# Kernel tuning notes

Measured on AMD Instinct MI355X. Metric: run time of the kernel, lower is better.

Reference implementation:

```python
import jax, jax.numpy as jnp
import numpy as np

B, L1, L2 = 4, 1024, 512
D_PG, D_EX = 2304, 1024
H, HKV, DH = 8, 4, 256
SCALE = 256.0 ** -0.5


def _rope(x, cos, sin):
    # x: [B, L, h, DH]; cos/sin: [B, L, 1, DH//2]
    x = x.astype(jnp.float32)
    x1, x2 = jnp.split(x, 2, axis=-1)
    return jnp.concatenate([x1 * cos - x2 * sin, x2 * cos + x1 * sin], axis=-1)


def setup_inputs() -> dict:
    key = jax.random.key(0)
    ks = jax.random.split(key, 16)
    s = 0.02
    return {
        "pg_embeds": jax.random.normal(ks[0], (B, L1, D_PG), jnp.float32),
        "ex_embeds": jax.random.normal(ks[1], (B, L2, D_EX), jnp.float32),
        "cos": jax.random.normal(ks[2], (B, L1 + L2, 1, DH // 2), jnp.float32),
        "sin": jax.random.normal(ks[3], (B, L1 + L2, 1, DH // 2), jnp.float32),
        "attention_mask": jnp.zeros((B, L1 + L2, L1 + L2), jnp.float32),
        "Wq0": jax.random.normal(ks[4], (H * DH, D_PG), jnp.float32) * s,
        "Wk0": jax.random.normal(ks[5], (HKV * DH, D_PG), jnp.float32) * s,
        "Wv0": jax.random.normal(ks[6], (HKV * DH, D_PG), jnp.float32) * s,
        "Wo0": jax.random.normal(ks[7], (D_PG, H * DH), jnp.float32) * s,
        "Wq1": jax.random.normal(ks[8], (H * DH, D_EX), jnp.float32) * s,
        "Wk1": jax.random.normal(ks[9], (HKV * DH, D_EX), jnp.float32) * s,
        "Wv1": jax.random.normal(ks[10], (HKV * DH, D_EX), jnp.float32) * s,
        "Wo1": jax.random.normal(ks[11], (D_EX, H * DH), jnp.float32) * s,
    }


def reference(pg_embeds, ex_embeds, cos, sin, attention_mask,
              Wq0, Wk0, Wv0, Wo0, Wq1, Wk1, Wv1, Wo1):
    b, l1 = pg_embeds.shape[0], pg_embeds.shape[1]
    l2 = ex_embeds.shape[1]
    # per-stream QKV projections, then concat along sequence
    q = jnp.concatenate([
        (pg_embeds @ Wq0.T).reshape(b, l1, H, DH),
        (ex_embeds @ Wq1.T).reshape(b, l2, H, DH)], axis=1)
    k = jnp.concatenate([
        (pg_embeds @ Wk0.T).reshape(b, l1, HKV, DH),
        (ex_embeds @ Wk1.T).reshape(b, l2, HKV, DH)], axis=1)
    v = jnp.concatenate([
        (pg_embeds @ Wv0.T).reshape(b, l1, HKV, DH),
        (ex_embeds @ Wv1.T).reshape(b, l2, HKV, DH)], axis=1)
    q = _rope(q, cos, sin)  # fp32
    k = _rope(k, cos, sin)
    # GQA: repeat KV heads to match query heads
    rep = H // HKV
    k = jnp.repeat(k, rep, axis=2)
    v = jnp.repeat(jnp.repeat(v, rep, axis=2).astype(jnp.float32), 1, axis=0)
    # scores: [B, H, L, L]
    scores = jnp.einsum('bqhd,bkhd->bhqk', q, k) * SCALE
    scores = scores + attention_mask[:, None, :, :]
    p = jax.nn.softmax(scores, axis=-1)
    att = jnp.einsum('bhqk,bkhd->bqhd', p, v).reshape(b, l1 + l2, H * DH)
    out0 = att[:, :l1] @ Wo0.T
    out1 = att[:, l1:] @ Wo1.T
    return (out0, out1)
```

## Files before the change

kernel.cpp:

```cpp
#include <hip/hip_runtime.h>
#include <stdint.h>
#include <stddef.h>


typedef _Float16 f16;
typedef _Float16 f16x8 __attribute__((ext_vector_type(8)));
typedef _Float16 f16x4 __attribute__((ext_vector_type(4)));
typedef float    f32x4 __attribute__((ext_vector_type(4)));

__device__ __forceinline__ void async_ld16(const void* g, void* l) {
  __builtin_amdgcn_global_load_lds((const __attribute__((address_space(1))) void*)g,
                                   (__attribute__((address_space(3))) void*)l,
                                   16, 0, 0);
}

template <typename Epi>
__device__ __forceinline__ void gemm256(f16* lds,
    const f16* __restrict__ A, int lda,
    const f16* __restrict__ B, int ldb,
    int K, Epi&& epi)
{
  const int t    = threadIdx.x;
  const int w    = t >> 6;
  const int lane = t & 63;
  const int q4   = lane >> 4;
  const int l16  = lane & 15;
  const int wm   = w >> 2;
  const int wn   = w & 3;

  f16* ldsA = lds;
  f16* ldsB = lds + 32768;

  const int scx = ((lane & 3) ^ ((lane >> 3) & 3)) * 8;
  const f16* aP = A + (size_t)(lane >> 2) * lda + scx;
  const f16* bP = B + (size_t)(lane >> 2) * ldb + scx;
  const size_t aR0 = (size_t)(w * 32) * lda;
  const size_t aR1 = aR0 + (size_t)16 * lda;
  const size_t bR0 = (size_t)(w * 32) * ldb;
  const size_t bR1 = bR0 + (size_t)16 * ldb;
  const int wo = w * 1024;

  const int sx = (l16 >> 1) & 3;
  const int arow = (wm * 128 + l16) * 32 + ((q4 ^ sx) * 8);
  const int brow = (wn * 64 + l16) * 32 + ((q4 ^ sx) * 8);

  f32x4 acc[8][4];
  const f32x4 vz = {0.f, 0.f, 0.f, 0.f};
#pragma unroll
  for (int i = 0; i < 8; ++i)
#pragma unroll
    for (int j = 0; j < 4; ++j) acc[i][j] = vz;

#pragma unroll
  for (int s = 0; s < 2; ++s) {
    const int kk = s * 32;
    async_ld16(aP + aR0 + kk, ldsA + s * 8192 + wo);
    async_ld16(aP + aR1 + kk, ldsA + s * 8192 + wo + 512);
    async_ld16(bP + bR0 + kk, ldsB + s * 8192 + wo);
    async_ld16(bP + bR1 + kk, ldsB + s * 8192 + wo + 512);
  }

  const int NT = K >> 6;
  for (int tk = 0; tk < NT; ++tk) {
    const int d  = (tk & 1) ? 16384 : 0;
    const int dn = 16384 - d;
    const bool st = tk + 1 < NT;
    const int kn = (tk + 1) << 6;
#pragma unroll
    for (int s = 0; s < 2; ++s) {
      if (s == 0 || st) asm volatile("s_waitcnt vmcnt(4)" ::: "memory");
      else              asm volatile("s_waitcnt vmcnt(0)" ::: "memory");
      asm volatile("s_barrier" ::: "memory");
      const f16* aS = ldsA + d + s * 8192;
      const f16* bS = ldsB + d + s * 8192;
      f16x8 af[8], bf[4];
#pragma unroll
      for (int i = 0; i < 8; ++i) af[i] = *(const f16x8*)(aS + arow + i * 512);
#pragma unroll
      for (int i = 0; i < 4; ++i) bf[i] = *(const f16x8*)(bS + brow + i * 512);
      if (st) {
        const int kk = kn + s * 32;
        async_ld16(aP + aR0 + kk, ldsA + dn + s * 8192 + wo);
        async_ld16(aP + aR1 + kk, ldsA + dn + s * 8192 + wo + 512);
        async_ld16(bP + bR0 + kk, ldsB + dn + s * 8192 + wo);
        async_ld16(bP + bR1 + kk, ldsB + dn + s * 8192 + wo + 512);
      }
      __builtin_amdgcn_s_setprio(1);
#pragma unroll
      for (int mi = 0; mi < 8; ++mi)
#pragma unroll
        for (int ni = 0; ni < 4; ++ni)
          acc[mi][ni] = __builtin_amdgcn_mfma_f32_16x16x32_f16(af[mi], bf[ni], acc[mi][ni], 0, 0, 0);
      __builtin_amdgcn_s_setprio(0);
      asm volatile("s_barrier" ::: "memory");
    }
  }

#pragma unroll
  for (int mi = 0; mi < 8; ++mi)
#pragma unroll
    for (int ni = 0; ni < 4; ++ni)
#pragma unroll
      for (int r = 0; r < 4; ++r)
        epi(wm * 128 + mi * 16 + q4 * 4 + r, wn * 64 + ni * 16 + l16, acc[mi][ni][r]);
}

template <typename Epi>
__device__ __forceinline__ void gemm_pipe(f16* lds,
    const f16* __restrict__ A, int lda,
    const f16* __restrict__ B, int ldb,
    int K, Epi&& epi)
{
  const int t    = threadIdx.x;
  const int w    = t >> 6;
  const int lane = t & 63;
  const int q4   = lane >> 4;
  const int l16  = lane & 15;
  const int wm   = w >> 1;
  const int wn   = w & 1;

  const int srow = w * 16 + (lane >> 2);
  const int scol = ((lane & 3) ^ ((lane >> 3) & 3)) * 8;
  const f16* aP = A + (size_t)srow * lda + scol;
  const f16* bP = B + (size_t)srow * ldb + scol;
  const size_t a128 = (size_t)128 * lda;
  const int wl = w * 512;

  const int sx = (l16 >> 1) & 3;
  const int arow = (wm * 64 + l16) * 32 + ((q4 ^ sx) * 8);
  const int brow = (wn * 64 + l16) * 32 + ((q4 ^ sx) * 8);

  f32x4 acc[4][4];
  const f32x4 vz = {0.f, 0.f, 0.f, 0.f};
#pragma unroll
  for (int i = 0; i < 4; ++i)
#pragma unroll
    for (int j = 0; j < 4; ++j) acc[i][j] = vz;

  async_ld16(aP,             lds + wl);
  async_ld16(aP + a128,      lds + 4096 + wl);
  async_ld16(bP,             lds + 32768 + wl);
  asm volatile("" ::: "memory");
  async_ld16(aP + 32,        lds + 8192 + wl);
  async_ld16(aP + a128 + 32, lds + 8192 + 4096 + wl);
  async_ld16(bP + 32,        lds + 32768 + 4096 + wl);
  asm volatile("s_waitcnt vmcnt(3)" ::: "memory");
  asm volatile("s_barrier" ::: "memory");

  const int NT = K >> 6;
  int cb = 0;
  for (int tk = 0; tk < NT; ++tk) {
    f16* aT = lds + cb * 16384;
    f16* bT = lds + 32768 + cb * 8192;
    f16* aD = lds + (cb ^ 1) * 16384;
    f16* bD = lds + 32768 + (cb ^ 1) * 8192;
    const int kn = (tk + 1) << 6;
    const bool st = tk < NT - 1;
#pragma unroll
    for (int s = 0; s < 2; ++s) {
      const f16* aS = aT + s * 8192;
      const f16* bS = bT + s * 4096;
      f16x8 af[4], bf[4];
#pragma unroll
      for (int i = 0; i < 4; ++i) {
        af[i] = *(const f16x8*)(aS + arow + i * 512);
        bf[i] = *(const f16x8*)(bS + brow + i * 512);
      }
      if (st) {
        if (s == 0) {
          async_ld16(aP + kn,        aD + wl);
          async_ld16(aP + a128 + kn, aD + 4096 + wl);
          async_ld16(bP + kn,        bD + wl);
        } else {
          async_ld16(aP + kn + 32,        aD + 8192 + wl);
          async_ld16(aP + a128 + kn + 32, aD + 8192 + 4096 + wl);
          async_ld16(bP + kn + 32,        bD + 4096 + wl);
        }
        asm volatile("s_waitcnt vmcnt(3)" ::: "memory");
      } else if (s == 0) {
        asm volatile("s_waitcnt vmcnt(0)" ::: "memory");
      }
      asm volatile("s_barrier" ::: "memory");
      __builtin_amdgcn_s_setprio(1);
#pragma unroll
      for (int mi = 0; mi < 4; ++mi)
#pragma unroll
        for (int ni = 0; ni < 4; ++ni)
          acc[mi][ni] = __builtin_amdgcn_mfma_f32_16x16x32_f16(af[mi], bf[ni], acc[mi][ni], 0, 0, 0);
      __builtin_amdgcn_s_setprio(0);
      asm volatile("s_barrier" ::: "memory");
    }
    cb ^= 1;
  }

#pragma unroll
  for (int mi = 0; mi < 4; ++mi)
#pragma unroll
    for (int ni = 0; ni < 4; ++ni)
#pragma unroll
      for (int r = 0; r < 4; ++r)
        epi(wm * 64 + mi * 16 + q4 * 4 + r, wn * 64 + ni * 16 + l16, acc[mi][ni][r]);
}

__global__ __launch_bounds__(512, 2) void k_qkv5(
    const f16* __restrict__ xpg, const f16* __restrict__ xex,
    const f16* __restrict__ W0,  const f16* __restrict__ W1,
    f16* __restrict__ q, f16* __restrict__ k, f16* __restrict__ v)
{
  __shared__ alignas(16) f16 lds[65536];
  const int idx = blockIdx.x;
  int by, bx, K; const f16 *A, *B;
  const bool s0 = idx < 256;
  if (s0) { by = idx >> 4; bx = idx & 15; K = 2304;
            A = xpg + (size_t)by * 256 * 2304; B = W0 + (size_t)bx * 256 * 2304; }
  else    { int j = idx - 256; by = j >> 4; bx = j & 15; K = 1024;
            A = xex + (size_t)by * 256 * 1024; B = W1 + (size_t)bx * 256 * 1024; }

  f16* D; int ldd, coff;
  if (bx < 8)       { D = q; ldd = 2048; coff = 0; }
  else if (bx < 12) { D = k; ldd = 1024; coff = 2048; }
  else              { D = v; ldd = 1024; coff = 3072; }
  const int colb = bx * 256 - coff;
  const int rowb = s0 ? ((by >> 2) * 1536 + (by & 3) * 256)
                      : ((by >> 1) * 1536 + 1024 + (by & 1) * 256);

  gemm256(lds, A, K, B, K, K, [&](int r, int c, float fv) {
    D[(size_t)(rowb + r) * ldd + colb + c] = (f16)fv;
  });
}

__global__ __launch_bounds__(256) void k_post(
    f16* __restrict__ q, f16* __restrict__ k,
    const float* __restrict__ cs, const float* __restrict__ sn,
    const float* __restrict__ msk, f16* __restrict__ mkh,
    const f16* __restrict__ v, f16* __restrict__ vt)
{
  const int blk = blockIdx.x;
  if (blk < 6144) {
    __shared__ f16 tile[32][33];
    const int b = blk / 1536, r0 = blk % 1536;
    const int d0 = (r0 & 31) * 32, l0 = (r0 >> 5) * 32;
    const int t = threadIdx.x;
    const int tr = t >> 5, tc = t & 31;
#pragma unroll
    for (int i = 0; i < 4; ++i)
      tile[tr + i * 8][tc] = v[((size_t)b * 1536 + l0 + tr + i * 8) * 1024 + d0 + tc];
    __syncthreads();
#pragma unroll
    for (int i = 0; i < 4; ++i) {
      int d = d0 + tr + i * 8;
      vt[(((size_t)b * 4 + (d >> 8)) * 256 + (d & 255)) * 1536 + l0 + tc] = tile[tc][tr + i * 8];
    }
  } else if (blk < 15360) {
    const size_t gid = ((size_t)(blk - 6144) * 256 + threadIdx.x) * 4;
    float4 m4 = *(const float4*)(msk + gid);
    f16x4 o = {(f16)m4.x, (f16)m4.y, (f16)m4.z, (f16)m4.w};
    *(f16x4*)(mkh + gid) = o;
  } else {
    const size_t tid8 = ((size_t)(blk - 15360) * 256 + threadIdx.x) * 8;
    f16* base; size_t row; int col;
    if (tid8 < 12582912ull) { base = q + tid8; row = tid8 >> 11; col = (int)(tid8 & 2047); }
    else { size_t f = tid8 - 12582912ull; base = k + f; row = f >> 10; col = (int)(f & 1023); }
    const int j0 = (col & 255) >> 1;
    f16x8 x = *(const f16x8*)base;
    float4 c4 = *(const float4*)(cs + row * 128 + j0);
    float4 s4 = *(const float4*)(sn + row * 128 + j0);
    f16x8 o;
    const float cc[4] = {c4.x, c4.y, c4.z, c4.w};
    const float ss[4] = {s4.x, s4.y, s4.z, s4.w};
#pragma unroll
    for (int p = 0; p < 4; ++p) {
      float x1 = (float)x[2 * p], x2 = (float)x[2 * p + 1];
      o[2 * p]     = (f16)(x1 * cc[p] - x2 * ss[p]);
      o[2 * p + 1] = (f16)(x2 * cc[p] + x1 * ss[p]);
    }
    *(f16x8*)base = o;
  }
}

__global__ __launch_bounds__(512, 2) void k_attn2(
    const f16* __restrict__ qb, const f16* __restrict__ kb,
    const f16* __restrict__ mask, f16* __restrict__ Sdst,
    const f16* __restrict__ Psrc, const f16* __restrict__ vt,
    f16* __restrict__ att0, f16* __restrict__ att1,
    const f16* __restrict__ wo0, const f16* __restrict__ wo1,
    float* __restrict__ out0, float* __restrict__ out1,
    int b_sc, int b_pv, int b_op, int npv, int nop)
{
  __shared__ alignas(16) f16 lds[49152];
  const int idx = blockIdx.x;
  if (idx < nop) {
    int by, bx, ldc, rowb; const f16 *A, *B; float* C;
    if (idx < 72) { by = idx / 18; bx = idx % 18;
                    A = att0 + (size_t)(b_op * 4 + by) * 256 * 2048;
                    B = wo0 + (size_t)bx * 128 * 2048;
                    C = out0; ldc = 2304; rowb = b_op * 1024 + by * 256; }
    else          { int j = idx - 72; by = j >> 3; bx = j & 7;
                    A = att1 + (size_t)(b_op * 2 + by) * 256 * 2048;
                    B = wo1 + (size_t)bx * 128 * 2048;
                    C = out1; ldc = 1024; rowb = b_op * 512 + by * 256; }
    const int colb = bx * 128;
    gemm_pipe(lds, A, 2048, B, 2048, 2048, [&](int r, int c, float fv) {
      C[(size_t)(rowb + r) * ldc + colb + c] = fv;
    });
  } else if (idx < nop + npv) {
    const int j = idx - nop;
    const int h = j / 12, rem = j % 12, by = rem >> 1, bx = rem & 1;
    const f16* A = Psrc + (size_t)h * 1536 * 1536 + (size_t)by * 256 * 1536;
    const f16* B = vt + (size_t)(b_pv * 4 + (h >> 1)) * 256 * 1536 + (size_t)bx * 128 * 1536;
    f16* dst = (by < 4)
      ? att0 + (size_t)(b_pv * 1024 + by * 256) * 2048 + h * 256 + bx * 128
      : att1 + (size_t)(b_pv * 512 + (by - 4) * 256) * 2048 + h * 256 + bx * 128;
    gemm_pipe(lds, A, 1536, B, 1536, 1536, [&](int r, int c, float fv) {
      dst[(size_t)r * 2048 + c] = (f16)fv;
    });
  } else {
    const int j = idx - nop - npv;
    const int h = j / 72, rem = j % 72, by = rem / 12, bx = rem % 12;
    const f16* A = qb + (size_t)b_sc * 1536 * 2048 + h * 256 + (size_t)by * 256 * 2048;
    const f16* B = kb + (size_t)b_sc * 1536 * 1024 + (h >> 1) * 256 + (size_t)bx * 128 * 1024;
    f16* Sz = Sdst + (size_t)h * 1536 * 1536 + (size_t)by * 256 * 1536 + bx * 128;
    const f16* mb = mask + (size_t)b_sc * 1536 * 1536 + (size_t)by * 256 * 1536 + bx * 128;
    gemm_pipe(lds, A, 2048, B, 1024, 256, [&](int r, int c, float fv) {
      size_t i = (size_t)r * 1536 + c;
      Sz[i] = (f16)(fv * 0.0625f + (float)mb[i]);
    });
  }
}

__global__ __launch_bounds__(256) void k_softmax(f16* __restrict__ S)
{
  const int row = blockIdx.x * 4 + (threadIdx.x >> 6);
  const int lane = threadIdx.x & 63;
  f16* p = S + (size_t)row * 1536 + lane * 8;
  f16x8 v0 = *(const f16x8*)p;
  f16x8 v1 = *(const f16x8*)(p + 512);
  f16x8 v2 = *(const f16x8*)(p + 1024);
  float x[24];
#pragma unroll
  for (int i = 0; i < 8; ++i) {
    x[i] = (float)v0[i]; x[8 + i] = (float)v1[i]; x[16 + i] = (float)v2[i];
  }
  float mx = x[0];
#pragma unroll
  for (int i = 1; i < 24; ++i) mx = fmaxf(mx, x[i]);
#pragma unroll
  for (int o = 32; o > 0; o >>= 1) mx = fmaxf(mx, __shfl_xor(mx, o, 64));
  float s = 0.f;
#pragma unroll
  for (int i = 0; i < 24; ++i) { x[i] = __expf(x[i] - mx); s += x[i]; }
#pragma unroll
  for (int o = 32; o > 0; o >>= 1) s += __shfl_xor(s, o, 64);
  const float inv = 1.f / s;
  f16x8 o0, o1, o2;
#pragma unroll
  for (int i = 0; i < 8; ++i) {
    o0[i] = (f16)(x[i] * inv); o1[i] = (f16)(x[8 + i] * inv); o2[i] = (f16)(x[16 + i] * inv);
  }
  *(f16x8*)p = o0; *(f16x8*)(p + 512) = o1; *(f16x8*)(p + 1024) = o2;
}

__global__ __launch_bounds__(256) void k_cast_all(
    const float* __restrict__ s0, const float* __restrict__ s1,
    const float* __restrict__ s2, const float* __restrict__ s3,
    const float* __restrict__ s4, const float* __restrict__ s5,
    f16* __restrict__ ws)
{
  const size_t gid = ((size_t)blockIdx.x * 256 + threadIdx.x) * 4;
  const float* s; size_t off, dst;
  if      (gid < 9437184ull)  { s = s0; off = gid;               dst = 0ull        + off; }
  else if (gid < 11534336ull) { s = s1; off = gid - 9437184ull;  dst = 9437184ull  + off; }
  else if (gid < 13893632ull) { s = s2; off = gid - 11534336ull; dst = 18612224ull + off; }
  else if (gid < 18612224ull) { s = s3; off = gid - 13893632ull; dst = 20971520ull + off; }
  else if (gid < 19660800ull) { s = s4; off = gid - 18612224ull; dst = 28835840ull + off; }
  else                        { s = s5; off = gid - 19660800ull; dst = 29884416ull + off; }
  float4 v = *(const float4*)(s + off);
  f16x4 o = {(f16)v.x, (f16)v.y, (f16)v.z, (f16)v.w};
  *(f16x4*)(ws + dst) = o;
}

__global__ __launch_bounds__(256) void k_cast_wr(
    const float* __restrict__ wq0, const float* __restrict__ wk0,
    const float* __restrict__ wq1, const float* __restrict__ wk1,
    f16* __restrict__ W0c, f16* __restrict__ W1c)
{
  const int idx = blockIdx.x;
  const float* src; f16* dstm; int K, r, drow;
  if      (idx < 2048) { src = wq0; dstm = W0c; K = 2304; r = idx;        drow = idx; }
  else if (idx < 3072) { src = wk0; dstm = W0c; K = 2304; r = idx - 2048; drow = idx; }
  else if (idx < 5120) { src = wq1; dstm = W1c; K = 1024; r = idx - 3072; drow = idx - 3072; }
  else                 { src = wk1; dstm = W1c; K = 1024; r = idx - 5120; drow = idx - 3072; }
  const int w = r & 255;
  const int srow = (r & ~255) + (w >> 1) + ((w & 1) << 7);
  const float* sp = src + (size_t)srow * K;
  f16* dp = dstm + (size_t)drow * K;
  for (int c = threadIdx.x * 4; c < K; c += 1024) {
    float4 v = *(const float4*)(sp + c);
    f16x4 o = {(f16)v.x, (f16)v.y, (f16)v.z, (f16)v.w};
    *(f16x4*)(dp + c) = o;
  }
}

extern "C" void kernel_launch(void* const* d_in, const int* in_sizes, int n_in,
                              void* d_out, int out_size, void* d_ws, size_t ws_size,
                              hipStream_t stream)
{
  (void)in_sizes; (void)n_in; (void)out_size; (void)ws_size;
  const float* pg  = (const float*)d_in[0];
  const float* ex  = (const float*)d_in[1];
  const float* cs  = (const float*)d_in[2];
  const float* sn  = (const float*)d_in[3];
  const float* msk = (const float*)d_in[4];

  char* ws = (char*)d_ws;
  f16* xpg  = (f16*)(ws + 0);
  f16* xex  = (f16*)(ws + 18874368);
  f16* W0c  = (f16*)(ws + 23068672);
  f16* wo0c = (f16*)(ws + 41943040);
  f16* W1c  = (f16*)(ws + 51380224);
  f16* wo1c = (f16*)(ws + 59768832);
  f16* qb   = (f16*)(ws + 63963136);
  f16* kb   = (f16*)(ws + 89128960);
  f16* vb   = (f16*)(ws + 101711872);
  f16* vt   = (f16*)(ws + 114294784);
  f16* att0 = (f16*)(ws + 126877696);
  f16* att1 = (f16*)(ws + 143654912);
  f16* S0   = (f16*)(ws + 152043520);
  f16* S1   = (f16*)(ws + 189792256);
  f16* mkh  = W0c;
  float* out0 = (float*)d_out;
  float* out1 = out0 + 9437184;

  k_cast_all<<<21248, 256, 0, stream>>>(
      pg, ex, (const float*)d_in[7], (const float*)d_in[8],
      (const float*)d_in[11], (const float*)d_in[12], (f16*)ws);
  k_cast_wr<<<6144, 256, 0, stream>>>(
      (const float*)d_in[5], (const float*)d_in[6],
      (const float*)d_in[9], (const float*)d_in[10], W0c, W1c);

  k_qkv5<<<384, 512, 0, stream>>>(xpg, xex, W0c, W1c, qb, kb, vb);

  k_post<<<24576, 256, 0, stream>>>(qb, kb, cs, sn, msk, mkh, vb, vt);

  k_attn2<<<576, 512, 0, stream>>>(qb, kb, mkh, S0, S0, vt, att0, att1, wo0c, wo1c, out0, out1, 0, 0, 0, 0, 0);
  k_softmax<<<3072, 256, 0, stream>>>(S0);
  k_attn2<<<672, 512, 0, stream>>>(qb, kb, mkh, S1, S0, vt, att0, att1, wo0c, wo1c, out0, out1, 1, 0, 0, 96, 0);
  k_softmax<<<3072, 256, 0, stream>>>(S1);
  k_attn2<<<760, 512, 0, stream>>>(qb, kb, mkh, S0, S1, vt, att0, att1, wo0c, wo1c, out0, out1, 2, 1, 0, 96, 88);
  k_softmax<<<3072, 256, 0, stream>>>(S0);
  k_attn2<<<760, 512, 0, stream>>>(qb, kb, mkh, S1, S0, vt, att0, att1, wo0c, wo1c, out0, out1, 3, 2, 1, 96, 88);
  k_softmax<<<3072, 256, 0, stream>>>(S1);

  k_attn2<<<184, 512, 0, stream>>>(qb, kb, mkh, S0, S1, vt, att0, att1, wo0c, wo1c, out0, out1, 0, 3, 2, 96, 88);
  k_attn2<<<88, 512, 0, stream>>>(qb, kb, mkh, S0, S1, vt, att0, att1, wo0c, wo1c, out0, out1, 0, 0, 3, 0, 88);
}
```

Measured before the change: 632.4 us.

## Split gemm256 K-step into four half-tile phases interleaving loads and MFMAs

Restructures the gemm256 main loop so each 32-wide K slice is handled in two phases: the first half of the A rows, then the second half. Global-to-LDS prefetches for A and B are spread across these phases, with waitcnt and barriers placed between them. The aim is finer-grained overlap of async loads, LDS reads and MFMA work, and fewer fragment registers live at once. The cost is more barriers per iteration and more intricate vmcnt accounting that could stall or race if a count is wrong.

Measured after the change: 630.7 us. No clear change (-0.3%).

```diff
diff --git a/kernel.cpp b/kernel.cpp
--- a/kernel.cpp
+++ b/kernel.cpp
@@ -51,14 +51,17 @@
 #pragma unroll
     for (int j = 0; j < 4; ++j) acc[i][j] = vz;
 
-#pragma unroll
-  for (int s = 0; s < 2; ++s) {
-    const int kk = s * 32;
-    async_ld16(aP + aR0 + kk, ldsA + s * 8192 + wo);
-    async_ld16(aP + aR1 + kk, ldsA + s * 8192 + wo + 512);
-    async_ld16(bP + bR0 + kk, ldsB + s * 8192 + wo);
-    async_ld16(bP + bR1 + kk, ldsB + s * 8192 + wo + 512);
-  }
+  async_ld16(aP + aR0, ldsA + wo);
+  async_ld16(aP + aR1, ldsA + wo + 512);
+  async_ld16(bP + bR0, ldsB + wo);
+  async_ld16(bP + bR1, ldsB + wo + 512);
+  asm volatile("" ::: "memory");
+  async_ld16(aP + aR0 + 32, ldsA + 8192 + wo);
+  async_ld16(aP + aR1 + 32, ldsA + 8192 + wo + 512);
+  async_ld16(bP + bR0 + 32, ldsB + 8192 + wo);
+  async_ld16(bP + bR1 + 32, ldsB + 8192 + wo + 512);
+  asm volatile("s_waitcnt vmcnt(4)" ::: "memory");
+  asm volatile("s_barrier" ::: "memory");
 
   const int NT = K >> 6;
   for (int tk = 0; tk < NT; ++tk) {
@@ -66,34 +69,85 @@
     const int dn = 16384 - d;
     const bool st = tk + 1 < NT;
     const int kn = (tk + 1) << 6;
-#pragma unroll
-    for (int s = 0; s < 2; ++s) {
-      if (s == 0 || st) asm volatile("s_waitcnt vmcnt(4)" ::: "memory");
-      else              asm volatile("s_waitcnt vmcnt(0)" ::: "memory");
-      asm volatile("s_barrier" ::: "memory");
-      const f16* aS = ldsA + d + s * 8192;
-      const f16* bS = ldsB + d + s * 8192;
-      f16x8 af[8], bf[4];
-#pragma unroll
-      for (int i = 0; i < 8; ++i) af[i] = *(const f16x8*)(aS + arow + i * 512);
-#pragma unroll
-      for (int i = 0; i < 4; ++i) bf[i] = *(const f16x8*)(bS + brow + i * 512);
-      if (st) {
-        const int kk = kn + s * 32;
-        async_ld16(aP + aR0 + kk, ldsA + dn + s * 8192 + wo);
-        async_ld16(aP + aR1 + kk, ldsA + dn + s * 8192 + wo + 512);
-        async_ld16(bP + bR0 + kk, ldsB + dn + s * 8192 + wo);
-        async_ld16(bP + bR1 + kk, ldsB + dn + s * 8192 + wo + 512);
-      }
-      __builtin_amdgcn_s_setprio(1);
-#pragma unroll
-      for (int mi = 0; mi < 8; ++mi)
-#pragma unroll
-        for (int ni = 0; ni < 4; ++ni)
-          acc[mi][ni] = __builtin_amdgcn_mfma_f32_16x16x32_f16(af[mi], bf[ni], acc[mi][ni], 0, 0, 0);
-      __builtin_amdgcn_s_setprio(0);
-      asm volatile("s_barrier" ::: "memory");
-    }
+    const f16* aS = ldsA + d;
+    const f16* bS = ldsB + d;
+    f16x8 a0[4], a1[4], bf[4];
+
+#pragma unroll
+    for (int i = 0; i < 4; ++i) {
+      a0[i] = *(const f16x8*)(aS + arow + i * 512);
+      bf[i] = *(const f16x8*)(bS + brow + i * 512);
+    }
+    if (st) {
+      async_ld16(aP + aR0 + kn, ldsA + dn + wo);
+      async_ld16(aP + aR1 + kn, ldsA + dn + wo + 512);
+    }
+    asm volatile("s_barrier" ::: "memory");
+    __builtin_amdgcn_s_setprio(1);
+#pragma unroll
+    for (int mi = 0; mi < 4; ++mi)
+#pragma unroll
+      for (int ni = 0; ni < 4; ++ni)
+        acc[mi][ni] = __builtin_amdgcn_mfma_f32_16x16x32_f16(a0[mi], bf[ni], acc[mi][ni], 0, 0, 0);
+    __builtin_amdgcn_s_setprio(0);
+    asm volatile("s_barrier" ::: "memory");
+
+#pragma unroll
+    for (int i = 0; i < 4; ++i)
+      a1[i] = *(const f16x8*)(aS + arow + (i + 4) * 512);
+    if (st) {
+      async_ld16(bP + bR0 + kn, ldsB + dn + wo);
+      async_ld16(bP + bR1 + kn, ldsB + dn + wo + 512);
+      asm volatile("s_waitcnt vmcnt(4)" ::: "memory");
+    } else {
+      asm volatile("s_waitcnt vmcnt(0)" ::: "memory");
+    }
+    asm volatile("s_barrier" ::: "memory");
+    __builtin_amdgcn_s_setprio(1);
+#pragma unroll
+    for (int mi = 0; mi < 4; ++mi)
+#pragma unroll
+      for (int ni = 0; ni < 4; ++ni)
+        acc[mi + 4][ni] = __builtin_amdgcn_mfma_f32_16x16x32_f16(a1[mi], bf[ni], acc[mi + 4][ni], 0, 0, 0);
+    __builtin_amdgcn_s_setprio(0);
+    asm volatile("s_barrier" ::: "memory");
+
+#pragma unroll
+    for (int i = 0; i < 4; ++i) {
+      a0[i] = *(const f16x8*)(aS + 8192 + arow + i * 512);
+      bf[i] = *(const f16x8*)(bS + 8192 + brow + i * 512);
+    }
+    if (st) {
+      async_ld16(aP + aR0 + kn + 32, ldsA + dn + 8192 + wo);
+      async_ld16(aP + aR1 + kn + 32, ldsA + dn + 8192 + wo + 512);
+    }
+    asm volatile("s_barrier" ::: "memory");
+    __builtin_amdgcn_s_setprio(1);
+#pragma unroll
+    for (int mi = 0; mi < 4; ++mi)
+#pragma unroll
+      for (int ni = 0; ni < 4; ++ni)
+        acc[mi][ni] = __builtin_amdgcn_mfma_f32_16x16x32_f16(a0[mi], bf[ni], acc[mi][ni], 0, 0, 0);
+    __builtin_amdgcn_s_setprio(0);
+    asm volatile("s_barrier" ::: "memory");
+
+#pragma unroll
+    for (int i = 0; i < 4; ++i)
+      a1[i] = *(const f16x8*)(aS + 8192 + arow + (i + 4) * 512);
+    if (st) {
+      async_ld16(bP + bR0 + kn + 32, ldsB + dn + 8192 + wo);
+      async_ld16(bP + bR1 + kn + 32, ldsB + dn + 8192 + wo + 512);
+      asm volatile("s_waitcnt vmcnt(4)" ::: "memory");
+    }
+    asm volatile("s_barrier" ::: "memory");
+    __builtin_amdgcn_s_setprio(1);
+#pragma unroll
+    for (int mi = 0; mi < 4; ++mi)
+#pragma unroll
+      for (int ni = 0; ni < 4; ++ni)
+        acc[mi + 4][ni] = __builtin_amdgcn_mfma_f32_16x16x32_f16(a1[mi], bf[ni], acc[mi + 4][ni], 0, 0, 0);
+    __builtin_amdgcn_s_setprio(0);
+    asm volatile("s_barrier" ::: "memory");
   }
 
 #pragma unroll
```
